# Performance work log

Hardware: AMD Instinct MI355X
Metric: run time of the kernel (lower is better)

## Reference

```python
import jax, jax.numpy as jnp
import numpy as np


def setup_inputs() -> dict:
    key = jax.random.key(0)
    k1, k2, k3 = jax.random.split(key, 3)
    batch, in_features, out_features = 4096, 8192, 8192
    x = jax.random.normal(k1, (batch, in_features), dtype=jnp.float32)
    weight = jax.random.normal(k2, (out_features, in_features), dtype=jnp.float32) * (1.0 / np.sqrt(in_features))
    bias = jax.random.normal(k3, (out_features,), dtype=jnp.float32) * (1.0 / np.sqrt(in_features))
    return {"x": x, "weight": weight, "bias": bias}


def reference(x, weight, bias):
    # Linear: [B, out] = x @ W^T + b
    y = jnp.einsum('bi,oi->bo', x, weight) + bias
    # Per-row sum over out_features, then mean (divide by out_features)
    mean_val = jnp.sum(y, axis=1) / weight.shape[0]  # [B]
    # Two logsumexp ops over a size-1 dim: log(exp(v)) twice == identity,
    # computed explicitly to match the original op chain.
    lse1 = jnp.log(jnp.exp(mean_val))
    lse2 = jnp.log(jnp.exp(lse1))
    return lse2[:, None]  # [B, 1]
```

## Files before the change

kernel.cpp:

```cpp
#include <hip/hip_runtime.h>

typedef float f32x4 __attribute__((ext_vector_type(4)));

constexpr int IN_F  = 8192;
constexpr int OUT_F = 8192;
constexpr int BATCH = 4096;
constexpr int TPB   = 256;

constexpr int COLG = IN_F / (TPB * 4);

__global__ __launch_bounds__(TPB) void colsum_kernel(
    const float* __restrict__ W, float* __restrict__ part, int rpc) {
    const int col4 = blockIdx.x * TPB + threadIdx.x;
    const f32x4* __restrict__ p = reinterpret_cast<const f32x4*>(W)
        + (long)blockIdx.y * rpc * (IN_F / 4) + col4;
    f32x4 acc = {0.f, 0.f, 0.f, 0.f};
    #pragma unroll 8
    for (int r = 0; r < rpc; ++r)
        acc += p[(long)r * (IN_F / 4)];
    reinterpret_cast<f32x4*>(part)[(long)blockIdx.y * (IN_F / 4) + col4] = acc;
}

__global__ __launch_bounds__(TPB) void combine_kernel(
    const float* __restrict__ part, const float* __restrict__ bias,
    float* __restrict__ wsum, float* __restrict__ bsum, int chunks) {
    const int blk = blockIdx.x, tid = threadIdx.x;
    if (blk < 32) {
        const int col = blk * TPB + tid;
        float s = 0.f;
        #pragma unroll 8
        for (int c = 0; c < chunks; ++c) s += part[(long)c * IN_F + col];
        wsum[col] = s;
    } else {
        __shared__ float red[4];
        float bs = 0.f;
        for (int k = tid; k < OUT_F; k += TPB) bs += bias[k];
        #pragma unroll
        for (int o = 32; o; o >>= 1) bs += __shfl_down(bs, o);
        if ((tid & 63) == 0) red[tid >> 6] = bs;
        __syncthreads();
        if (tid == 0) *bsum = red[0] + red[1] + red[2] + red[3];
    }
}

constexpr int NBLK_R = 2048;
constexpr int ROWS_R = BATCH / NBLK_R;

__global__ __launch_bounds__(TPB) void rowdot_kernel(
    const float* __restrict__ x, const float* __restrict__ wsum,
    const float* __restrict__ bsum, float* __restrict__ out) {
    __shared__ float red[8];
    const int tid = threadIdx.x;
    const long rowbase = (long)blockIdx.x * ROWS_R;
    const f32x4* __restrict__ x4 =
        reinterpret_cast<const f32x4*>(x) + rowbase * (IN_F / 4);
    const f32x4* __restrict__ w4 = reinterpret_cast<const f32x4*>(wsum);

    float s0 = 0.f, s1 = 0.f;
    #pragma unroll
    for (int k = tid; k < IN_F / 4; k += TPB) {
        f32x4 wv = w4[k];
        f32x4 a  = x4[k];
        f32x4 b  = x4[(IN_F / 4) + k];
        s0 += a.x * wv.x + a.y * wv.y + a.z * wv.z + a.w * wv.w;
        s1 += b.x * wv.x + b.y * wv.y + b.z * wv.z + b.w * wv.w;
    }
    #pragma unroll
    for (int o = 32; o; o >>= 1) {
        s0 += __shfl_down(s0, o);
        s1 += __shfl_down(s1, o);
    }
    const int wid = tid >> 6;
    if ((tid & 63) == 0) { red[wid] = s0; red[4 + wid] = s1; }
    __syncthreads();
    if (tid == 0) {
        const float bsv = *bsum;
        out[rowbase]     = (red[0] + red[1] + red[2] + red[3] + bsv) * (1.0f / OUT_F);
        out[rowbase + 1] = (red[4] + red[5] + red[6] + red[7] + bsv) * (1.0f / OUT_F);
    }
}

extern "C" void kernel_launch(void* const* d_in, const int* in_sizes, int n_in,
                              void* d_out, int out_size, void* d_ws, size_t ws_size,
                              hipStream_t stream) {
    const float* x    = (const float*)d_in[0];
    const float* W    = (const float*)d_in[1];
    const float* bias = (const float*)d_in[2];
    float*       out  = (float*)d_out;

    int chunks = 256;
    while (chunks > 1 &&
           ((size_t)chunks * IN_F + IN_F + 16) * sizeof(float) > ws_size)
        chunks >>= 1;
    const int rpc = OUT_F / chunks;

    float* part = (float*)d_ws;
    float* wsum = part + (size_t)chunks * IN_F;
    float* bsum = wsum + IN_F;

    colsum_kernel<<<dim3(COLG, chunks), TPB, 0, stream>>>(W, part, rpc);
    combine_kernel<<<33, TPB, 0, stream>>>(part, bias, wsum, bsum, chunks);
    rowdot_kernel<<<NBLK_R, TPB, 0, stream>>>(x, wsum, bsum, out);
}
```

Baseline: 100.7 us.

## Fuse colsum, combine and rowdot into one cooperative kernel with grid syncs

Merges the three kernels (weight column sums, partial combine plus bias sum, and the row dot product) into a single cooperative launch of 2048 blocks that uses two grid-wide barriers between phases. This removes two kernel launch gaps and lets phases start without host-side dependency handling. It falls back to the original three-kernel path if cooperative launch or enough resident blocks are not available. The risks are grid.sync overhead, the occupancy query and attribute calls on every launch, and idle blocks during the 33-block combine phase.

```diff
diff --git a/kernel.cpp b/kernel.cpp
--- a/kernel.cpp
+++ b/kernel.cpp
@@ -1,4 +1,7 @@
 #include <hip/hip_runtime.h>
+#include <hip/hip_cooperative_groups.h>
+
+namespace cg = cooperative_groups;
 
 typedef float f32x4 __attribute__((ext_vector_type(4)));
 
@@ -6,6 +9,82 @@
 constexpr int OUT_F = 8192;
 constexpr int BATCH = 4096;
 constexpr int TPB   = 256;
+
+constexpr int NBLK   = 2048;
+constexpr int CHUNKS = NBLK / 8;
+constexpr int RPC    = OUT_F / CHUNKS;
+constexpr int ROWS   = BATCH / NBLK;
+
+__global__ __launch_bounds__(TPB, 8) void fused_kernel(
+    const float* __restrict__ x, const float* __restrict__ W,
+    const float* __restrict__ bias, float* __restrict__ out,
+    float* __restrict__ part, float* __restrict__ wsum,
+    float* __restrict__ bsum) {
+
+    __shared__ float red[8];
+    const int tid = threadIdx.x, blk = blockIdx.x;
+
+    {
+        const int g = blk & 7;
+        const int c = blk >> 3;
+        const f32x4* __restrict__ p = reinterpret_cast<const f32x4*>(W)
+            + (long)c * RPC * (IN_F / 4) + g * TPB + tid;
+        f32x4 acc = {0.f, 0.f, 0.f, 0.f};
+        #pragma unroll 8
+        for (int r = 0; r < RPC; ++r)
+            acc += p[(long)r * (IN_F / 4)];
+        reinterpret_cast<f32x4*>(part)[(long)c * (IN_F / 4) + g * TPB + tid] = acc;
+    }
+
+    cg::this_grid().sync();
+
+    if (blk < 32) {
+        const int col = blk * TPB + tid;
+        float s = 0.f;
+        #pragma unroll 8
+        for (int c = 0; c < CHUNKS; ++c) s += part[(long)c * IN_F + col];
+        wsum[col] = s;
+    } else if (blk == 32) {
+        float bs = 0.f;
+        for (int k = tid; k < OUT_F; k += TPB) bs += bias[k];
+        #pragma unroll
+        for (int o = 32; o; o >>= 1) bs += __shfl_down(bs, o);
+        if ((tid & 63) == 0) red[tid >> 6] = bs;
+        __syncthreads();
+        if (tid == 0) *bsum = red[0] + red[1] + red[2] + red[3];
+    }
+
+    cg::this_grid().sync();
+
+    {
+        const long rowbase = (long)blk * ROWS;
+        const f32x4* __restrict__ x4 =
+            reinterpret_cast<const f32x4*>(x) + rowbase * (IN_F / 4);
+        const f32x4* __restrict__ w4 = reinterpret_cast<const f32x4*>(wsum);
+        float s0 = 0.f, s1 = 0.f;
+        #pragma unroll
+        for (int k = tid; k < IN_F / 4; k += TPB) {
+            f32x4 wv = w4[k];
+            f32x4 a  = x4[k];
+            f32x4 b  = x4[(IN_F / 4) + k];
+            s0 += a.x * wv.x + a.y * wv.y + a.z * wv.z + a.w * wv.w;
+            s1 += b.x * wv.x + b.y * wv.y + b.z * wv.z + b.w * wv.w;
+        }
+        #pragma unroll
+        for (int o = 32; o; o >>= 1) {
+            s0 += __shfl_down(s0, o);
+            s1 += __shfl_down(s1, o);
+        }
+        const int wid = tid >> 6;
+        if ((tid & 63) == 0) { red[wid] = s0; red[4 + wid] = s1; }
+        __syncthreads();
+        if (tid == 0) {
+            const float bsv = *bsum;
+            out[rowbase]     = (red[0]+red[1]+red[2]+red[3] + bsv) * (1.0f / OUT_F);
+            out[rowbase + 1] = (red[4]+red[5]+red[6]+red[7] + bsv) * (1.0f / OUT_F);
+        }
+    }
+}
 
 constexpr int COLG = IN_F / (TPB * 4);
 
@@ -43,19 +122,15 @@
     }
 }
 
-constexpr int NBLK_R = 2048;
-constexpr int ROWS_R = BATCH / NBLK_R;
-
 __global__ __launch_bounds__(TPB) void rowdot_kernel(
     const float* __restrict__ x, const float* __restrict__ wsum,
     const float* __restrict__ bsum, float* __restrict__ out) {
     __shared__ float red[8];
     const int tid = threadIdx.x;
-    const long rowbase = (long)blockIdx.x * ROWS_R;
+    const long rowbase = (long)blockIdx.x * ROWS;
     const f32x4* __restrict__ x4 =
         reinterpret_cast<const f32x4*>(x) + rowbase * (IN_F / 4);
     const f32x4* __restrict__ w4 = reinterpret_cast<const f32x4*>(wsum);
-
     float s0 = 0.f, s1 = 0.f;
     #pragma unroll
     for (int k = tid; k < IN_F / 4; k += TPB) {
@@ -75,8 +150,8 @@
     __syncthreads();
     if (tid == 0) {
         const float bsv = *bsum;
-        out[rowbase]     = (red[0] + red[1] + red[2] + red[3] + bsv) * (1.0f / OUT_F);
-        out[rowbase + 1] = (red[4] + red[5] + red[6] + red[7] + bsv) * (1.0f / OUT_F);
+        out[rowbase]     = (red[0]+red[1]+red[2]+red[3] + bsv) * (1.0f / OUT_F);
+        out[rowbase + 1] = (red[4]+red[5]+red[6]+red[7] + bsv) * (1.0f / OUT_F);
     }
 }
 
@@ -88,17 +163,33 @@
     const float* bias = (const float*)d_in[2];
     float*       out  = (float*)d_out;
 
+    float* part = (float*)d_ws;
+    float* wsum = part + (size_t)CHUNKS * IN_F;
+    float* bsum = wsum + IN_F;
+
+    int dev = 0;    (void)hipGetDevice(&dev);
+    int coop = 0;   (void)hipDeviceGetAttribute(&coop, hipDeviceAttributeCooperativeLaunch, dev);
+    int ncu = 0;    (void)hipDeviceGetAttribute(&ncu, hipDeviceAttributeMultiprocessorCount, dev);
+    int maxblk = 0;
+    (void)hipOccupancyMaxActiveBlocksPerMultiprocessor(&maxblk, fused_kernel, TPB, 0);
+
+    if (coop && (long)maxblk * ncu >= NBLK &&
+        ((size_t)CHUNKS * IN_F + IN_F + 16) * sizeof(float) <= ws_size) {
+        void* args[] = {(void*)&x, (void*)&W, (void*)&bias, (void*)&out,
+                        (void*)&part, (void*)&wsum, (void*)&bsum};
+        hipError_t err = hipLaunchCooperativeKernel(
+            (const void*)fused_kernel, dim3(NBLK), dim3(TPB), args, 0, stream);
+        if (err == hipSuccess) return;
+    }
+
     int chunks = 256;
     while (chunks > 1 &&
            ((size_t)chunks * IN_F + IN_F + 16) * sizeof(float) > ws_size)
         chunks >>= 1;
     const int rpc = OUT_F / chunks;
-
-    float* part = (float*)d_ws;
-    float* wsum = part + (size_t)chunks * IN_F;
-    float* bsum = wsum + IN_F;
-
+    float* wsumF = part + (size_t)chunks * IN_F;
+    float* bsumF = wsumF + IN_F;
     colsum_kernel<<<dim3(COLG, chunks), TPB, 0, stream>>>(W, part, rpc);
-    combine_kernel<<<33, TPB, 0, stream>>>(part, bias, wsum, bsum, chunks);
-    rowdot_kernel<<<NBLK_R, TPB, 0, stream>>>(x, wsum, bsum, out);
+    combine_kernel<<<33, TPB, 0, stream>>>(part, bias, wsumF, bsumF, chunks);
+    rowdot_kernel<<<BATCH / ROWS, TPB, 0, stream>>>(x, wsumF, bsumF, out);
 }
```

Measured after the change: 100.3 us. Within noise of the previous version (-0.4%).
